# Optimization experiments

Measured on AMD Instinct MI355X. Metric: run time of the kernel, lower is better.

Reference implementation:

```python
import jax, jax.numpy as jnp
import numpy as np
from jax import lax

B, L, N_NODES, N_SEQ = 256, 15360, 16, 64


def _lstm_layer(x, wih, whh, bih, bhh):
    # x: (B, T, I); torch gate order i, f, g, o
    H = whh.shape[1]
    b = bih + bhh
    def step(carry, xt):
        h, c = carry
        gates = xt @ wih.T + h @ whh.T + b
        i, f, g, o = jnp.split(gates, 4, axis=-1)
        c = jax.nn.sigmoid(f) * c + jax.nn.sigmoid(i) * jnp.tanh(g)
        h = jax.nn.sigmoid(o) * jnp.tanh(c)
        return (h, c), h
    h0 = jnp.zeros((x.shape[0], H), x.dtype)
    _, ys = lax.scan(step, (h0, h0), x.transpose(1, 0, 2))
    return ys.transpose(1, 0, 2)


def setup_inputs() -> dict:
    ks = iter(jax.random.split(jax.random.key(0), 64))
    def rn(shape, scale=1.0):
        return (jax.random.normal(next(ks), shape) * scale).astype(jnp.float32)
    d = {"x": rn((B, 1, L))}
    chs = [1, 16, 32, 64]
    for i in range(3):
        cin, cout = chs[i], chs[i + 1]
        s = 1.0 / np.sqrt(cin * 5)
        d[f"cw{i}"] = rn((cout, cin, 5), s)
        d[f"cb{i}"] = rn((cout,), s)
        d[f"bng{i}"] = jnp.ones((cout,), jnp.float32)
        d[f"bnb{i}"] = jnp.zeros((cout,), jnp.float32)
        d[f"bnm{i}"] = jnp.zeros((cout,), jnp.float32)
        d[f"bnv{i}"] = jnp.ones((cout,), jnp.float32)
    Hh = 64
    for l in range(2):
        s = 1.0 / np.sqrt(Hh)
        d[f"wih{l}"] = rn((4 * Hh, 64), s)
        d[f"whh{l}"] = rn((4 * Hh, Hh), s)
        d[f"bih{l}"] = rn((4 * Hh,), s)
        d[f"bhh{l}"] = rn((4 * Hh,), s)
    gin = [256, 64, 64]
    for l in range(3):
        s = 1.0 / np.sqrt(gin[l])
        d[f"gw{l}"] = rn((64, gin[l]), s)
        d[f"gb{l}"] = rn((64,), s)
    d["clw"] = rn((5, 64), 0.125)
    d["clb"] = rn((5,), 0.125)
    return d


def reference(x, cw0, cb0, bng0, bnb0, bnm0, bnv0, cw1, cb1, bng1, bnb1, bnm1, bnv1, cw2, cb2, bng2, bnb2, bnm2, bnv2, wih0, whh0, bih0, bhh0, wih1, whh1, bih1, bhh1, gw0, gb0, gw1, gb1, gw2, gb2, clw, clb):
    h = x
    # CNN: [Conv1d(k=5,p=2) -> BN(eval) -> ReLU -> MaxPool(2)] x 3
    for cw, cb, g, b, m, v in ((cw0, cb0, bng0, bnb0, bnm0, bnv0),
                               (cw1, cb1, bng1, bnb1, bnm1, bnv1),
                               (cw2, cb2, bng2, bnb2, bnm2, bnv2)):
        h = lax.conv_general_dilated(h, cw, (1,), [(2, 2)], dimension_numbers=("NCH", "OIH", "NCH")) + cb[None, :, None]
        h = g[None, :, None] * (h - m[None, :, None]) * lax.rsqrt(v[None, :, None] + 1e-5) + b[None, :, None]
        h = jax.nn.relu(h)
        Bq, Cq, Lq = h.shape
        h = h.reshape(Bq, Cq, Lq // 2, 2).max(-1)
    # AdaptiveAvgPool1d(64): length divisible by 64 -> exact mean bins
    Bq, Cq, Lq = h.shape
    h = h.reshape(Bq, Cq, N_SEQ, Lq // N_SEQ).mean(-1)
    h = h.transpose(0, 2, 1)  # (B, 64, 64) = (batch, seq, channels)
    # 2-layer LSTM (dropout is identity in eval)
    h = _lstm_layer(h, wih0, whh0, bih0, bhh0)
    h = _lstm_layer(h, wih1, whh1, bih1, bhh1)
    # Graph builder: Pearson-style correlation + value thresholding
    Hf = h.reshape(Bq, -1)
    fpn = Hf.shape[1] // N_NODES  # 256 features per node
    nf = Hf[:, :N_NODES * fpn].reshape(Bq, N_NODES, fpn)
    cen = nf - nf.mean(-1, keepdims=True)
    nrm = cen / (jnp.std(cen, axis=-1, ddof=1, keepdims=True) + 1e-8)
    C = jnp.einsum("bnf,bmf->bnm", nrm, nrm) / fpn  # (B, N, N)
    Cf = C.reshape(Bq, -1)
    k = min(max(1, int((100.0 - 25.0) / 100.0 * Cf.shape[1])), Cf.shape[1] - 1)
    thr = jnp.sort(Cf, axis=1)[:, k - 1]  # torch.kthvalue(k)
    eye = jnp.eye(N_NODES, dtype=C.dtype)
    adj = (C > thr[:, None, None]).astype(C.dtype) * (1.0 - eye)
    # GCN: x = ReLU(W (x + A x) + b), 3 layers, then max over nodes
    g = nf
    for gw, gb in ((gw0, gb0), (gw1, gb1), (gw2, gb2)):
        g = jax.nn.relu((g + jnp.einsum("bnm,bmf->bnf", adj, g)) @ gw.T + gb)
    emb = g.max(axis=1)
    return emb @ clw.T + clb
```

## Files before the change

kernel.cpp:

```cpp
#include <hip/hip_runtime.h>
#include <math.h>

typedef __attribute__((ext_vector_type(2))) float v2f;

__global__ __launch_bounds__(256) void prep_weights_kernel(
    const float* __restrict__ cw0, const float* __restrict__ cb0,
    const float* __restrict__ bng0, const float* __restrict__ bnb0,
    const float* __restrict__ bnm0, const float* __restrict__ bnv0,
    const float* __restrict__ cw1, const float* __restrict__ cb1,
    const float* __restrict__ bng1, const float* __restrict__ bnb1,
    const float* __restrict__ bnm1, const float* __restrict__ bnv1,
    const float* __restrict__ cw2, const float* __restrict__ cb2,
    const float* __restrict__ bng2, const float* __restrict__ bnb2,
    const float* __restrict__ bnm2, const float* __restrict__ bnv2,
    float* __restrict__ wt1, float* __restrict__ b1,
    float* __restrict__ wt2, float* __restrict__ b2,
    float* __restrict__ w0f, float* __restrict__ b0f)
{
    int tid = threadIdx.x;
    for (int i = tid; i < 2560; i += 256) {
        int co = i & 31, r = i >> 5, t = r % 5, ci = r / 5;
        float s = bng1[co] * rsqrtf(bnv1[co] + 1e-5f);
        wt1[i] = cw1[(co * 16 + ci) * 5 + t] * s;
    }
    if (tid < 32) {
        float s = bng1[tid] * rsqrtf(bnv1[tid] + 1e-5f);
        b1[tid] = (cb1[tid] - bnm1[tid]) * s + bnb1[tid];
    }
    for (int i = tid; i < 10240; i += 256) {
        int co = i & 63, r = i >> 6, t = r % 5, ci = r / 5;
        float s = bng2[co] * rsqrtf(bnv2[co] + 1e-5f);
        wt2[i] = cw2[(co * 32 + ci) * 5 + t] * s;
    }
    if (tid < 64) {
        float s = bng2[tid] * rsqrtf(bnv2[tid] + 1e-5f);
        b2[tid] = (cb2[tid] - bnm2[tid]) * s + bnb2[tid];
    }
    if (tid < 80) {
        int co = tid / 5;
        float s = bng0[co] * rsqrtf(bnv0[co] + 1e-5f);
        w0f[tid] = cw0[tid] * s;
    }
    if (tid < 16) {
        float s = bng0[tid] * rsqrtf(bnv0[tid] + 1e-5f);
        b0f[tid] = (cb0[tid] - bnm0[tid]) * s + bnb0[tid];
    }
}

__global__ __launch_bounds__(256) void convall_kernel(
    const float* __restrict__ x,
    const float* __restrict__ w0f, const float* __restrict__ b0f,
    const float* __restrict__ wt1, const float* __restrict__ b1,
    const float* __restrict__ wt2, const float* __restrict__ b2,
    float* __restrict__ xs)
{
    __shared__ float raw[512];
    __shared__ float U[8320];
    int b = blockIdx.y, bx = blockIdx.x, tid = threadIdx.x;
    const float* xb = x + (size_t)b * 15360;
    {
        int base = 480 * bx - 14;
        for (int i = tid; i < 508; i += 256) {
            int g = base + i;
            raw[i] = (g >= 0 && g < 15360) ? xb[g] : 0.f;
        }
    }
    __syncthreads();
    {
        int ci0 = tid >> 4, sub = tid & 15;
        float w0 = w0f[ci0*5+0], w1 = w0f[ci0*5+1], w2 = w0f[ci0*5+2],
              w3 = w0f[ci0*5+3], w4 = w0f[ci0*5+4];
        float bb = b0f[ci0];
        int r0g = 240 * bx - 6;
        for (int p = sub; p < 252; p += 16) {
            int r = r0g + p;
            float v = 0.f;
            if (r >= 0 && r < 7680) {
                int i0 = 2 * p;
                float c0 = raw[i0],   c1 = raw[i0+1], c2 = raw[i0+2],
                      c3 = raw[i0+3], c4 = raw[i0+4], c5 = raw[i0+5];
                float s0 = fmaf(w0,c0, fmaf(w1,c1, fmaf(w2,c2, fmaf(w3,c3, w4*c4))));
                float s1 = fmaf(w0,c1, fmaf(w1,c2, fmaf(w2,c3, fmaf(w3,c4, w4*c5))));
                v = fmaxf(fmaxf(s0, s1) + bb, 0.f);
            }
            U[ci0 * 256 + p] = v;
        }
    }
    __syncthreads();
    {
        int cg = tid >> 7, jj = tid & 127;
        int cgu = __builtin_amdgcn_readfirstlane(cg);
        { int co = tid >> 3, c = 124 + (tid & 7); U[4096 + co * 132 + c] = 0.f; }
        if (jj < 124) {
            const float* wb = wt1 + cgu * 16;
            v2f a0[8], a1[8];
#pragma unroll
            for (int q = 0; q < 8; ++q) { a0[q] = (v2f){0.f,0.f}; a1[q] = (v2f){0.f,0.f}; }
#pragma unroll 4
            for (int ci = 0; ci < 16; ++ci) {
                const float2* xr = reinterpret_cast<const float2*>(&U[ci * 256]);
                float2 xA = xr[jj], xB = xr[jj + 1], xC = xr[jj + 2];
                float xv[6] = { xA.x, xA.y, xB.x, xB.y, xC.x, xC.y };
#pragma unroll
                for (int t = 0; t < 5; ++t) {
                    const v2f* wp2 = reinterpret_cast<const v2f*>(wb + (ci * 5 + t) * 32);
                    v2f va = { xv[t], xv[t] };
                    v2f vc = { xv[t + 1], xv[t + 1] };
#pragma unroll
                    for (int q2 = 0; q2 < 8; ++q2) {
                        v2f w = wp2[q2];
                        a0[q2] = __builtin_elementwise_fma(w, va, a0[q2]);
                        a1[q2] = __builtin_elementwise_fma(w, vc, a1[q2]);
                    }
                }
            }
            int q = 120 * bx - 2 + jj;
            bool ok = (q >= 0 && q < 3840);
#pragma unroll
            for (int q2 = 0; q2 < 8; ++q2) {
#pragma unroll
                for (int cpp = 0; cpp < 2; ++cpp) {
                    int qq = 2 * q2 + cpp;
                    int co = cgu * 16 + qq;
                    float val = 0.f;
                    if (ok) val = fmaxf(fmaxf(a0[q2][cpp], a1[q2][cpp]) + b1[co], 0.f);
                    U[4096 + co * 132 + jj] = val;
                }
            }
        }
    }
    __syncthreads();
    {
        int cg = tid >> 6, jj = tid & 63;
        int cgu = __builtin_amdgcn_readfirstlane(cg);
        const float* wb = wt2 + cgu * 16;
        v2f a0[8], a1[8];
#pragma unroll
        for (int q = 0; q < 8; ++q) { a0[q] = (v2f){0.f,0.f}; a1[q] = (v2f){0.f,0.f}; }
#pragma unroll 4
        for (int ci = 0; ci < 32; ++ci) {
            const float2* xr = reinterpret_cast<const float2*>(&U[4096 + ci * 132]);
            float2 xA = xr[jj], xB = xr[jj + 1], xC = xr[jj + 2];
            float xv[6] = { xA.x, xA.y, xB.x, xB.y, xC.x, xC.y };
#pragma unroll
            for (int t = 0; t < 5; ++t) {
                const v2f* wp2 = reinterpret_cast<const v2f*>(wb + (ci * 5 + t) * 64);
                v2f va = { xv[t], xv[t] };
                v2f vc = { xv[t + 1], xv[t + 1] };
#pragma unroll
                for (int q2 = 0; q2 < 8; ++q2) {
                    v2f w = wp2[q2];
                    a0[q2] = __builtin_elementwise_fma(w, va, a0[q2]);
                    a1[q2] = __builtin_elementwise_fma(w, vc, a1[q2]);
                }
            }
        }
        __syncthreads();
        if (jj < 60) {
#pragma unroll
            for (int q2 = 0; q2 < 8; ++q2) {
#pragma unroll
                for (int cpp = 0; cpp < 2; ++cpp) {
                    int qq = 2 * q2 + cpp;
                    int co = cgu * 16 + qq;
                    float m = fmaxf(a0[q2][cpp], a1[q2][cpp]) + b2[co];
                    U[co * 61 + jj] = fmaxf(m, 0.f);
                }
            }
        }
    }
    __syncthreads();
    if (tid < 128) {
        int co = tid & 63, bin = tid >> 6;
        const float* r = U + co * 61 + bin * 30;
        float s = 0.f;
#pragma unroll
        for (int k = 0; k < 30; ++k) s += r[k];
        xs[((size_t)b * 64 + (bx * 2 + bin)) * 64 + co] = s * (1.f / 30.f);
    }
}

__global__ __launch_bounds__(256) void lstm_kernel(
    const float* __restrict__ xseq,
    const float* __restrict__ wih0, const float* __restrict__ whh0,
    const float* __restrict__ bih0, const float* __restrict__ bhh0,
    const float* __restrict__ wih1, const float* __restrict__ whh1,
    const float* __restrict__ bih1, const float* __restrict__ bhh1,
    float* __restrict__ hseq)
{
    __shared__ float xb[64][64];
    __shared__ float xg[64][256];
    __shared__ float gb4[4][64];
    __shared__ float hb[64];
    int b = blockIdx.x;
    int tid = threadIdx.x;
    int wv = tid >> 6, ln = tid & 63;
    for (int i = tid; i < 4096; i += 256) xb[i >> 6][i & 63] = xseq[(size_t)b * 4096 + i];
    __syncthreads();
    float wr[64];
    for (int layer = 0; layer < 2; ++layer) {
        const float* wih = layer ? wih1 : wih0;
        const float* whh = layer ? whh1 : whh0;
        float bias = layer ? (bih1[tid] + bhh1[tid]) : (bih0[tid] + bhh0[tid]);
#pragma unroll
        for (int k4 = 0; k4 < 16; ++k4) {
            float4 v = reinterpret_cast<const float4*>(wih + (size_t)tid * 64)[k4];
            wr[k4 * 4 + 0] = v.x; wr[k4 * 4 + 1] = v.y;
            wr[k4 * 4 + 2] = v.z; wr[k4 * 4 + 3] = v.w;
        }
        for (int t = 0; t < 64; ++t) {
            float s0 = bias, s1 = 0.f, s2 = 0.f, s3 = 0.f;
#pragma unroll
            for (int k4 = 0; k4 < 16; ++k4) {
                float4 xv4 = *reinterpret_cast<const float4*>(&xb[t][k4 * 4]);
                s0 = fmaf(wr[k4 * 4 + 0], xv4.x, s0);
                s1 = fmaf(wr[k4 * 4 + 1], xv4.y, s1);
                s2 = fmaf(wr[k4 * 4 + 2], xv4.z, s2);
                s3 = fmaf(wr[k4 * 4 + 3], xv4.w, s3);
            }
            xg[t][tid] = (s0 + s1) + (s2 + s3);
        }
#pragma unroll
        for (int k4 = 0; k4 < 16; ++k4) {
            float4 v = reinterpret_cast<const float4*>(whh + (size_t)tid * 64)[k4];
            wr[k4 * 4 + 0] = v.x; wr[k4 * 4 + 1] = v.y;
            wr[k4 * 4 + 2] = v.z; wr[k4 * 4 + 3] = v.w;
        }
        if (tid < 64) hb[tid] = 0.f;
        float c = 0.f;
        __syncthreads();
        for (int t = 0; t < 64; ++t) {
            float s0 = xg[t][tid], s1 = 0.f, s2 = 0.f, s3 = 0.f;
#pragma unroll
            for (int k4 = 0; k4 < 16; ++k4) {
                float4 hv4 = *reinterpret_cast<const float4*>(&hb[k4 * 4]);
                s0 = fmaf(wr[k4 * 4 + 0], hv4.x, s0);
                s1 = fmaf(wr[k4 * 4 + 1], hv4.y, s1);
                s2 = fmaf(wr[k4 * 4 + 2], hv4.z, s2);
                s3 = fmaf(wr[k4 * 4 + 3], hv4.w, s3);
            }
            float acc = (s0 + s1) + (s2 + s3);
            float a;
            if (wv == 2) a = tanhf(acc);
            else         a = 1.f / (1.f + __expf(-acc));
            gb4[wv][ln] = a;
            __syncthreads();
            float gi = gb4[0][ln], gf = gb4[1][ln], gg = gb4[2][ln], go = gb4[3][ln];
            c = fmaf(gf, c, gi * gg);
            float h = go * tanhf(c);
            if (wv == 0) {
                hb[ln] = h;
                if (layer == 0) xb[t][ln] = h;
                else hseq[((size_t)b * 64 + t) * 64 + ln] = h;
            }
            __syncthreads();
        }
    }
}

__global__ __launch_bounds__(256) void graph_kernel(
    const float* __restrict__ hseq,
    const float* __restrict__ gw0, const float* __restrict__ gb0,
    const float* __restrict__ gw1, const float* __restrict__ gb1,
    const float* __restrict__ gw2, const float* __restrict__ gb2,
    const float* __restrict__ clw, const float* __restrict__ clb,
    float* __restrict__ out)
{
    __shared__ float nf[16][257];
    __shared__ float sb[16][257];
    __shared__ float red[16][17];
    __shared__ float mean[16], rstd[16];
    __shared__ float C[256];
    __shared__ float adj[16][16];
    __shared__ float thrv;
    __shared__ float bufA[16][65], bufB[16][65], bufC[16][65];
    __shared__ float emb[64];
    int b = blockIdx.x, tid = threadIdx.x;
    for (int i = tid; i < 4096; i += 256) nf[i >> 8][i & 255] = hseq[(size_t)b * 4096 + i];
    __syncthreads();
    int nd = tid >> 4, sub = tid & 15;
    {
        float s = 0.f;
        for (int f = sub; f < 256; f += 16) s += nf[nd][f];
        red[nd][sub] = s;
    }
    __syncthreads();
    if (tid < 16) {
        float m = 0.f;
        for (int i = 0; i < 16; ++i) m += red[tid][i];
        mean[tid] = m * (1.f / 256.f);
    }
    __syncthreads();
    {
        float mu = mean[nd];
        float ss = 0.f;
        for (int f = sub; f < 256; f += 16) { float d = nf[nd][f] - mu; ss = fmaf(d, d, ss); }
        red[nd][sub] = ss;
    }
    __syncthreads();
    if (tid < 16) {
        float m = 0.f;
        for (int i = 0; i < 16; ++i) m += red[tid][i];
        rstd[tid] = 1.f / (sqrtf(m * (1.f / 255.f)) + 1e-8f);
    }
    __syncthreads();
    for (int i = tid; i < 4096; i += 256) {
        int n = i >> 8, f = i & 255;
        sb[n][f] = (nf[n][f] - mean[n]) * rstd[n];
    }
    __syncthreads();
    {
        int n = tid >> 4, m = tid & 15;
        float a0 = 0, a1 = 0, a2 = 0, a3 = 0;
        for (int f = 0; f < 256; f += 4) {
            a0 = fmaf(sb[n][f + 0], sb[m][f + 0], a0);
            a1 = fmaf(sb[n][f + 1], sb[m][f + 1], a1);
            a2 = fmaf(sb[n][f + 2], sb[m][f + 2], a2);
            a3 = fmaf(sb[n][f + 3], sb[m][f + 3], a3);
        }
        C[tid] = ((a0 + a1) + (a2 + a3)) * (1.f / 256.f);
    }
    __syncthreads();
    {
        float v = C[tid];
        int cnt = 0, eq = 0;
        for (int j2 = 0; j2 < 256; ++j2) {
            float vj = C[j2];
            cnt += (vj < v);
            eq  += (vj == v);
        }
        if (cnt <= 191 && 191 < cnt + eq) thrv = v;
    }
    __syncthreads();
    {
        int n = tid >> 4, m = tid & 15;
        adj[n][m] = (C[tid] > thrv && n != m) ? 1.f : 0.f;
    }
    __syncthreads();
    for (int i = tid; i < 4096; i += 256) {
        int n = i >> 8, f = i & 255;
        float acc = nf[n][f];
#pragma unroll
        for (int m = 0; m < 16; ++m) acc = fmaf(adj[n][m], nf[m][f], acc);
        sb[n][f] = acc;
    }
    __syncthreads();
    for (int i = tid; i < 1024; i += 256) {
        int n = i >> 6, o = i & 63;
        const float4* wr4 = reinterpret_cast<const float4*>(gw0 + (size_t)o * 256);
        float acc = gb0[o];
        for (int f4 = 0; f4 < 64; ++f4) {
            float4 wv = wr4[f4];
            int f = f4 * 4;
            acc = fmaf(sb[n][f + 0], wv.x, acc);
            acc = fmaf(sb[n][f + 1], wv.y, acc);
            acc = fmaf(sb[n][f + 2], wv.z, acc);
            acc = fmaf(sb[n][f + 3], wv.w, acc);
        }
        bufA[n][o] = fmaxf(acc, 0.f);
    }
    __syncthreads();
    for (int i = tid; i < 1024; i += 256) {
        int n = i >> 6, f = i & 63;
        float acc = bufA[n][f];
#pragma unroll
        for (int m = 0; m < 16; ++m) acc = fmaf(adj[n][m], bufA[m][f], acc);
        bufB[n][f] = acc;
    }
    __syncthreads();
    for (int i = tid; i < 1024; i += 256) {
        int n = i >> 6, o = i & 63;
        const float4* wr4 = reinterpret_cast<const float4*>(gw1 + (size_t)o * 64);
        float acc = gb1[o];
        for (int f4 = 0; f4 < 16; ++f4) {
            float4 wv = wr4[f4];
            int f = f4 * 4;
            acc = fmaf(bufB[n][f + 0], wv.x, acc);
            acc = fmaf(bufB[n][f + 1], wv.y, acc);
            acc = fmaf(bufB[n][f + 2], wv.z, acc);
            acc = fmaf(bufB[n][f + 3], wv.w, acc);
        }
        bufC[n][o] = fmaxf(acc, 0.f);
    }
    __syncthreads();
    for (int i = tid; i < 1024; i += 256) {
        int n = i >> 6, f = i & 63;
        float acc = bufC[n][f];
#pragma unroll
        for (int m = 0; m < 16; ++m) acc = fmaf(adj[n][m], bufC[m][f], acc);
        bufA[n][f] = acc;
    }
    __syncthreads();
    for (int i = tid; i < 1024; i += 256) {
        int n = i >> 6, o = i & 63;
        const float4* wr4 = reinterpret_cast<const float4*>(gw2 + (size_t)o * 64);
        float acc = gb2[o];
        for (int f4 = 0; f4 < 16; ++f4) {
            float4 wv = wr4[f4];
            int f = f4 * 4;
            acc = fmaf(bufA[n][f + 0], wv.x, acc);
            acc = fmaf(bufA[n][f + 1], wv.y, acc);
            acc = fmaf(bufA[n][f + 2], wv.z, acc);
            acc = fmaf(bufA[n][f + 3], wv.w, acc);
        }
        bufB[n][o] = fmaxf(acc, 0.f);
    }
    __syncthreads();
    if (tid < 64) {
        float mx = bufB[0][tid];
#pragma unroll
        for (int n = 1; n < 16; ++n) mx = fmaxf(mx, bufB[n][tid]);
        emb[tid] = mx;
    }
    __syncthreads();
    if (tid < 5) {
        float acc = clb[tid];
#pragma unroll
        for (int o = 0; o < 64; ++o) acc = fmaf(emb[o], clw[tid * 64 + o], acc);
        out[(size_t)b * 5 + tid] = acc;
    }
}

extern "C" void kernel_launch(void* const* d_in, const int* in_sizes, int n_in,
                              void* d_out, int out_size, void* d_ws, size_t ws_size,
                              hipStream_t stream)
{
    const float* x    = (const float*)d_in[0];
    const float* cw0  = (const float*)d_in[1];
    const float* cb0  = (const float*)d_in[2];
    const float* bng0 = (const float*)d_in[3];
    const float* bnb0 = (const float*)d_in[4];
    const float* bnm0 = (const float*)d_in[5];
    const float* bnv0 = (const float*)d_in[6];
    const float* cw1  = (const float*)d_in[7];
    const float* cb1  = (const float*)d_in[8];
    const float* bng1 = (const float*)d_in[9];
    const float* bnb1 = (const float*)d_in[10];
    const float* bnm1 = (const float*)d_in[11];
    const float* bnv1 = (const float*)d_in[12];
    const float* cw2  = (const float*)d_in[13];
    const float* cb2  = (const float*)d_in[14];
    const float* bng2 = (const float*)d_in[15];
    const float* bnb2 = (const float*)d_in[16];
    const float* bnm2 = (const float*)d_in[17];
    const float* bnv2 = (const float*)d_in[18];
    const float* wih0 = (const float*)d_in[19];
    const float* whh0 = (const float*)d_in[20];
    const float* bih0 = (const float*)d_in[21];
    const float* bhh0 = (const float*)d_in[22];
    const float* wih1 = (const float*)d_in[23];
    const float* whh1 = (const float*)d_in[24];
    const float* bih1 = (const float*)d_in[25];
    const float* bhh1 = (const float*)d_in[26];
    const float* gw0  = (const float*)d_in[27];
    const float* gb0  = (const float*)d_in[28];
    const float* gw1  = (const float*)d_in[29];
    const float* gb1  = (const float*)d_in[30];
    const float* gw2  = (const float*)d_in[31];
    const float* gb2  = (const float*)d_in[32];
    const float* clw  = (const float*)d_in[33];
    const float* clb  = (const float*)d_in[34];

    float* xs  = (float*)d_ws;
    float* hs  = xs + 1048576;
    float* wt1 = hs + 1048576;
    float* b1  = wt1 + 2560;
    float* wt2 = b1 + 32;
    float* b2  = wt2 + 10240;
    float* w0f = b2 + 64;
    float* b0f = w0f + 80;

    prep_weights_kernel<<<1, 256, 0, stream>>>(
        cw0, cb0, bng0, bnb0, bnm0, bnv0,
        cw1, cb1, bng1, bnb1, bnm1, bnv1,
        cw2, cb2, bng2, bnb2, bnm2, bnv2,
        wt1, b1, wt2, b2, w0f, b0f);
    convall_kernel<<<dim3(32, 256), 256, 0, stream>>>(x, w0f, b0f, wt1, b1, wt2, b2, xs);
    lstm_kernel<<<256, 256, 0, stream>>>(xs, wih0, whh0, bih0, bhh0,
                                         wih1, whh1, bih1, bhh1, hs);
    graph_kernel<<<256, 256, 0, stream>>>(hs, gw0, gb0, gw1, gb1, gw2, gb2,
                                          clw, clb, (float*)d_out);
}
```

Baseline: 478.0 us.

## Fuse LSTM and graph kernels, remove per-step barrier, shrink conv LDS

Merges the LSTM and graph/GCN kernels into one, so the layer-2 hidden sequence stays in shared memory and the global round trip and a launch go away. Each wave now keeps its own copy of h and double-buffers the gate buffer, which drops the second __syncthreads per timestep. The conv kernel packs its shared buffers tighter (raw aliased into U, smaller strides, clamped reads) to use less LDS and possibly raise occupancy. The tighter strides may add bank conflicts, and the merged kernel's larger shared footprint may lower occupancy.

After: 469.0 us. No clear change (-1.9%).

```diff
diff --git a/kernel.cpp b/kernel.cpp
--- a/kernel.cpp
+++ b/kernel.cpp
@@ -54,8 +54,8 @@
     const float* __restrict__ wt2, const float* __restrict__ b2,
     float* __restrict__ xs)
 {
-    __shared__ float raw[512];
-    __shared__ float U[8320];
+    __shared__ float U[8096];
+    float* raw = &U[4064];
     int b = blockIdx.y, bx = blockIdx.x, tid = threadIdx.x;
     const float* xb = x + (size_t)b * 15360;
     {
@@ -83,14 +83,14 @@
                 float s1 = fmaf(w0,c1, fmaf(w1,c2, fmaf(w2,c3, fmaf(w3,c4, w4*c5))));
                 v = fmaxf(fmaxf(s0, s1) + bb, 0.f);
             }
-            U[ci0 * 256 + p] = v;
+            U[ci0 * 254 + p] = v;
         }
     }
     __syncthreads();
     {
         int cg = tid >> 7, jj = tid & 127;
         int cgu = __builtin_amdgcn_readfirstlane(cg);
-        { int co = tid >> 3, c = 124 + (tid & 7); U[4096 + co * 132 + c] = 0.f; }
+        if (tid < 64) { int co = tid >> 1, c = 124 + (tid & 1); U[4064 + co * 126 + c] = 0.f; }
         if (jj < 124) {
             const float* wb = wt1 + cgu * 16;
             v2f a0[8], a1[8];
@@ -98,7 +98,7 @@
             for (int q = 0; q < 8; ++q) { a0[q] = (v2f){0.f,0.f}; a1[q] = (v2f){0.f,0.f}; }
 #pragma unroll 4
             for (int ci = 0; ci < 16; ++ci) {
-                const float2* xr = reinterpret_cast<const float2*>(&U[ci * 256]);
+                const float2* xr = reinterpret_cast<const float2*>(&U[ci * 254]);
                 float2 xA = xr[jj], xB = xr[jj + 1], xC = xr[jj + 2];
                 float xv[6] = { xA.x, xA.y, xB.x, xB.y, xC.x, xC.y };
 #pragma unroll
@@ -124,7 +124,7 @@
                     int co = cgu * 16 + qq;
                     float val = 0.f;
                     if (ok) val = fmaxf(fmaxf(a0[q2][cpp], a1[q2][cpp]) + b1[co], 0.f);
-                    U[4096 + co * 132 + jj] = val;
+                    U[4064 + co * 126 + jj] = val;
                 }
             }
         }
@@ -132,6 +132,7 @@
     __syncthreads();
     {
         int cg = tid >> 6, jj = tid & 63;
+        int jje = (jj < 59) ? jj : 59;
         int cgu = __builtin_amdgcn_readfirstlane(cg);
         const float* wb = wt2 + cgu * 16;
         v2f a0[8], a1[8];
@@ -139,8 +140,8 @@
         for (int q = 0; q < 8; ++q) { a0[q] = (v2f){0.f,0.f}; a1[q] = (v2f){0.f,0.f}; }
 #pragma unroll 4
         for (int ci = 0; ci < 32; ++ci) {
-            const float2* xr = reinterpret_cast<const float2*>(&U[4096 + ci * 132]);
-            float2 xA = xr[jj], xB = xr[jj + 1], xC = xr[jj + 2];
+            const float2* xr = reinterpret_cast<const float2*>(&U[4064 + ci * 126]);
+            float2 xA = xr[jje], xB = xr[jje + 1], xC = xr[jje + 2];
             float xv[6] = { xA.x, xA.y, xB.x, xB.y, xC.x, xC.y };
 #pragma unroll
             for (int t = 0; t < 5; ++t) {
@@ -176,22 +177,26 @@
         float s = 0.f;
 #pragma unroll
         for (int k = 0; k < 30; ++k) s += r[k];
-        xs[((size_t)b * 64 + (bx * 2 + bin)) * 64 + co] = s * (1.f / 30.f);
+        xs[((size_t)b * 64 + (blockIdx.x * 2 + bin)) * 64 + co] = s * (1.f / 30.f);
     }
 }
 
-__global__ __launch_bounds__(256) void lstm_kernel(
+__global__ __launch_bounds__(256) void lstmgraph_kernel(
     const float* __restrict__ xseq,
     const float* __restrict__ wih0, const float* __restrict__ whh0,
     const float* __restrict__ bih0, const float* __restrict__ bhh0,
     const float* __restrict__ wih1, const float* __restrict__ whh1,
     const float* __restrict__ bih1, const float* __restrict__ bhh1,
-    float* __restrict__ hseq)
+    const float* __restrict__ gw0, const float* __restrict__ gb0,
+    const float* __restrict__ gw1, const float* __restrict__ gb1,
+    const float* __restrict__ gw2, const float* __restrict__ gb2,
+    const float* __restrict__ clw, const float* __restrict__ clb,
+    float* __restrict__ out)
 {
     __shared__ float xb[64][64];
-    __shared__ float xg[64][256];
-    __shared__ float gb4[4][64];
-    __shared__ float hb[64];
+    __shared__ float xg[16384];
+    __shared__ float gbuf[2][4][64];
+    __shared__ float hbw[4][64];
     int b = blockIdx.x;
     int tid = threadIdx.x;
     int wv = tid >> 6, ln = tid & 63;
@@ -218,7 +223,7 @@
                 s2 = fmaf(wr[k4 * 4 + 2], xv4.z, s2);
                 s3 = fmaf(wr[k4 * 4 + 3], xv4.w, s3);
             }
-            xg[t][tid] = (s0 + s1) + (s2 + s3);
+            xg[t * 256 + tid] = (s0 + s1) + (s2 + s3);
         }
 #pragma unroll
         for (int k4 = 0; k4 < 16; ++k4) {
@@ -226,14 +231,14 @@
             wr[k4 * 4 + 0] = v.x; wr[k4 * 4 + 1] = v.y;
             wr[k4 * 4 + 2] = v.z; wr[k4 * 4 + 3] = v.w;
         }
-        if (tid < 64) hb[tid] = 0.f;
+        hbw[wv][ln] = 0.f;
         float c = 0.f;
         __syncthreads();
         for (int t = 0; t < 64; ++t) {
-            float s0 = xg[t][tid], s1 = 0.f, s2 = 0.f, s3 = 0.f;
+            float s0 = xg[t * 256 + tid], s1 = 0.f, s2 = 0.f, s3 = 0.f;
 #pragma unroll
             for (int k4 = 0; k4 < 16; ++k4) {
-                float4 hv4 = *reinterpret_cast<const float4*>(&hb[k4 * 4]);
+                float4 hv4 = *reinterpret_cast<const float4*>(&hbw[wv][k4 * 4]);
                 s0 = fmaf(wr[k4 * 4 + 0], hv4.x, s0);
                 s1 = fmaf(wr[k4 * 4 + 1], hv4.y, s1);
                 s2 = fmaf(wr[k4 * 4 + 2], hv4.z, s2);
@@ -243,80 +248,73 @@
             float a;
             if (wv == 2) a = tanhf(acc);
             else         a = 1.f / (1.f + __expf(-acc));
-            gb4[wv][ln] = a;
+            gbuf[t & 1][wv][ln] = a;
             __syncthreads();
-            float gi = gb4[0][ln], gf = gb4[1][ln], gg = gb4[2][ln], go = gb4[3][ln];
+            float gi = gbuf[t & 1][0][ln], gf = gbuf[t & 1][1][ln],
+                  gg = gbuf[t & 1][2][ln], go = gbuf[t & 1][3][ln];
             c = fmaf(gf, c, gi * gg);
             float h = go * tanhf(c);
-            if (wv == 0) {
-                hb[ln] = h;
-                if (layer == 0) xb[t][ln] = h;
-                else hseq[((size_t)b * 64 + t) * 64 + ln] = h;
-            }
-            __syncthreads();
-        }
-    }
-}
-
-__global__ __launch_bounds__(256) void graph_kernel(
-    const float* __restrict__ hseq,
-    const float* __restrict__ gw0, const float* __restrict__ gb0,
-    const float* __restrict__ gw1, const float* __restrict__ gb1,
-    const float* __restrict__ gw2, const float* __restrict__ gb2,
-    const float* __restrict__ clw, const float* __restrict__ clb,
-    float* __restrict__ out)
-{
-    __shared__ float nf[16][257];
-    __shared__ float sb[16][257];
-    __shared__ float red[16][17];
-    __shared__ float mean[16], rstd[16];
-    __shared__ float C[256];
-    __shared__ float adj[16][16];
-    __shared__ float thrv;
-    __shared__ float bufA[16][65], bufB[16][65], bufC[16][65];
-    __shared__ float emb[64];
-    int b = blockIdx.x, tid = threadIdx.x;
-    for (int i = tid; i < 4096; i += 256) nf[i >> 8][i & 255] = hseq[(size_t)b * 4096 + i];
+            hbw[wv][ln] = h;
+            if (wv == 0) xb[t][ln] = h;
+        }
+        __syncthreads();
+    }
+    float* nf   = xg;
+    float* sb   = xg + 4112;
+    float* red  = xg + 8224;
+    float* mean = xg + 8496;
+    float* rstd = xg + 8512;
+    float* C    = xg + 8528;
+    float* adj  = xg + 8784;
+    float* thrv = xg + 9040;
+    float* bufA = xg + 9044;
+    float* bufB = xg + 10084;
+    float* bufC = xg + 11124;
+    float* emb  = xg + 12164;
+    for (int i = tid; i < 4096; i += 256) {
+        int n = i >> 8, f = i & 255;
+        nf[n * 257 + f] = xb[4 * n + (f >> 6)][f & 63];
+    }
     __syncthreads();
     int nd = tid >> 4, sub = tid & 15;
     {
         float s = 0.f;
-        for (int f = sub; f < 256; f += 16) s += nf[nd][f];
-        red[nd][sub] = s;
+        for (int f = sub; f < 256; f += 16) s += nf[nd * 257 + f];
+        red[nd * 17 + sub] = s;
     }
     __syncthreads();
     if (tid < 16) {
         float m = 0.f;
-        for (int i = 0; i < 16; ++i) m += red[tid][i];
+        for (int i = 0; i < 16; ++i) m += red[tid * 17 + i];
         mean[tid] = m * (1.f / 256.f);
     }
     __syncthreads();
     {
         float mu = mean[nd];
         float ss = 0.f;
-        for (int f = sub; f < 256; f += 16) { float d = nf[nd][f] - mu; ss = fmaf(d, d, ss); }
-        red[nd][sub] = ss;
+        for (int f = sub; f < 256; f += 16) { float d = nf[nd * 257 + f] - mu; ss = fmaf(d, d, ss); }
+        red[nd * 17 + sub] = ss;
     }
     __syncthreads();
     if (tid < 16) {
         float m = 0.f;
-        for (int i = 0; i < 16; ++i) m += red[tid][i];
+        for (int i = 0; i < 16; ++i) m += red[tid * 17 + i];
         rstd[tid] = 1.f / (sqrtf(m * (1.f / 255.f)) + 1e-8f);
     }
     __syncthreads();
     for (int i = tid; i < 4096; i += 256) {
         int n = i >> 8, f = i & 255;
-        sb[n][f] = (nf[n][f] - mean[n]) * rstd[n];
+        sb[n * 257 + f] = (nf[n * 257 + f] - mean[n]) * rstd[n];
     }
     __syncthreads();
     {
         int n = tid >> 4, m = tid & 15;
         float a0 = 0, a1 = 0, a2 = 0, a3 = 0;
         for (int f = 0; f < 256; f += 4) {
-            a0 = fmaf(sb[n][f + 0], sb[m][f + 0], a0);
-            a1 = fmaf(sb[n][f + 1], sb[m][f + 1], a1);
-            a2 = fmaf(sb[n][f + 2], sb[m][f + 2], a2);
-            a3 = fmaf(sb[n][f + 3], sb[m][f + 3], a3);
+            a0 = fmaf(sb[n * 257 + f + 0], sb[m * 257 + f + 0], a0);
+            a1 = fmaf(sb[n * 257 + f + 1], sb[m * 257 + f + 1], a1);
+            a2 = fmaf(sb[n * 257 + f + 2], sb[m * 257 + f + 2], a2);
+            a3 = fmaf(sb[n * 257 + f + 3], sb[m * 257 + f + 3], a3);
         }
         C[tid] = ((a0 + a1) + (a2 + a3)) * (1.f / 256.f);
     }
@@ -329,20 +327,20 @@
             cnt += (vj < v);
             eq  += (vj == v);
         }
-        if (cnt <= 191 && 191 < cnt + eq) thrv = v;
+        if (cnt <= 191 && 191 < cnt + eq) thrv[0] = v;
     }
     __syncthreads();
     {
         int n = tid >> 4, m = tid & 15;
-        adj[n][m] = (C[tid] > thrv && n != m) ? 1.f : 0.f;
+        adj[tid] = (C[tid] > thrv[0] && n != m) ? 1.f : 0.f;
     }
     __syncthreads();
     for (int i = tid; i < 4096; i += 256) {
         int n = i >> 8, f = i & 255;
-        float acc = nf[n][f];
-#pragma unroll
-        for (int m = 0; m < 16; ++m) acc = fmaf(adj[n][m], nf[m][f], acc);
-        sb[n][f] = acc;
+        float acc = nf[n * 257 + f];
+#pragma unroll
+        for (int m = 0; m < 16; ++m) acc = fmaf(adj[n * 16 + m], nf[m * 257 + f], acc);
+        sb[n * 257 + f] = acc;
     }
     __syncthreads();
     for (int i = tid; i < 1024; i += 256) {
@@ -350,22 +348,22 @@
         const float4* wr4 = reinterpret_cast<const float4*>(gw0 + (size_t)o * 256);
         float acc = gb0[o];
         for (int f4 = 0; f4 < 64; ++f4) {
-            float4 wv = wr4[f4];
+            float4 wv4 = wr4[f4];
             int f = f4 * 4;
-            acc = fmaf(sb[n][f + 0], wv.x, acc);
-            acc = fmaf(sb[n][f + 1], wv.y, acc);
-            acc = fmaf(sb[n][f + 2], wv.z, acc);
-            acc = fmaf(sb[n][f + 3], wv.w, acc);
-        }
-        bufA[n][o] = fmaxf(acc, 0.f);
+            acc = fmaf(sb[n * 257 + f + 0], wv4.x, acc);
+            acc = fmaf(sb[n * 257 + f + 1], wv4.y, acc);
+            acc = fmaf(sb[n * 257 + f + 2], wv4.z, acc);
+            acc = fmaf(sb[n * 257 + f + 3], wv4.w, acc);
+        }
+        bufA[n * 65 + o] = fmaxf(acc, 0.f);
     }
     __syncthreads();
     for (int i = tid; i < 1024; i += 256) {
         int n = i >> 6, f = i & 63;
-        float acc = bufA[n][f];
-#pragma unroll
-        for (int m = 0; m < 16; ++m) acc = fmaf(adj[n][m], bufA[m][f], acc);
-        bufB[n][f] = acc;
+        float acc = bufA[n * 65 + f];
+#pragma unroll
+        for (int m = 0; m < 16; ++m) acc = fmaf(adj[n * 16 + m], bufA[m * 65 + f], acc);
+        bufB[n * 65 + f] = acc;
     }
     __syncthreads();
     for (int i = tid; i < 1024; i += 256) {
@@ -373,22 +371,22 @@
         const float4* wr4 = reinterpret_cast<const float4*>(gw1 + (size_t)o * 64);
         float acc = gb1[o];
         for (int f4 = 0; f4 < 16; ++f4) {
-            float4 wv = wr4[f4];
+            float4 wv4 = wr4[f4];
             int f = f4 * 4;
-            acc = fmaf(bufB[n][f + 0], wv.x, acc);
-            acc = fmaf(bufB[n][f + 1], wv.y, acc);
-            acc = fmaf(bufB[n][f + 2], wv.z, acc);
-            acc = fmaf(bufB[n][f + 3], wv.w, acc);
-        }
-        bufC[n][o] = fmaxf(acc, 0.f);
+            acc = fmaf(bufB[n * 65 + f + 0], wv4.x, acc);
+            acc = fmaf(bufB[n * 65 + f + 1], wv4.y, acc);
+            acc = fmaf(bufB[n * 65 + f + 2], wv4.z, acc);
+            acc = fmaf(bufB[n * 65 + f + 3], wv4.w, acc);
+        }
+        bufC[n * 65 + o] = fmaxf(acc, 0.f);
     }
     __syncthreads();
     for (int i = tid; i < 1024; i += 256) {
         int n = i >> 6, f = i & 63;
-        float acc = bufC[n][f];
-#pragma unroll
-        for (int m = 0; m < 16; ++m) acc = fmaf(adj[n][m], bufC[m][f], acc);
-        bufA[n][f] = acc;
+        float acc = bufC[n * 65 + f];
+#pragma unroll
+        for (int m = 0; m < 16; ++m) acc = fmaf(adj[n * 16 + m], bufC[m * 65 + f], acc);
+        bufA[n * 65 + f] = acc;
     }
     __syncthreads();
     for (int i = tid; i < 1024; i += 256) {
@@ -396,20 +394,20 @@
         const float4* wr4 = reinterpret_cast<const float4*>(gw2 + (size_t)o * 64);
         float acc = gb2[o];
         for (int f4 = 0; f4 < 16; ++f4) {
-            float4 wv = wr4[f4];
+            float4 wv4 = wr4[f4];
             int f = f4 * 4;
-            acc = fmaf(bufA[n][f + 0], wv.x, acc);
-            acc = fmaf(bufA[n][f + 1], wv.y, acc);
-            acc = fmaf(bufA[n][f + 2], wv.z, acc);
-            acc = fmaf(bufA[n][f + 3], wv.w, acc);
-        }
-        bufB[n][o] = fmaxf(acc, 0.f);
+            acc = fmaf(bufA[n * 65 + f + 0], wv4.x, acc);
+            acc = fmaf(bufA[n * 65 + f + 1], wv4.y, acc);
+            acc = fmaf(bufA[n * 65 + f + 2], wv4.z, acc);
+            acc = fmaf(bufA[n * 65 + f + 3], wv4.w, acc);
+        }
+        bufB[n * 65 + o] = fmaxf(acc, 0.f);
     }
     __syncthreads();
     if (tid < 64) {
-        float mx = bufB[0][tid];
-#pragma unroll
-        for (int n = 1; n < 16; ++n) mx = fmaxf(mx, bufB[n][tid]);
+        float mx = bufB[0 * 65 + tid];
+#pragma unroll
+        for (int n = 1; n < 16; ++n) mx = fmaxf(mx, bufB[n * 65 + tid]);
         emb[tid] = mx;
     }
     __syncthreads();
@@ -462,8 +460,7 @@
     const float* clb  = (const float*)d_in[34];
 
     float* xs  = (float*)d_ws;
-    float* hs  = xs + 1048576;
-    float* wt1 = hs + 1048576;
+    float* wt1 = xs + 1048576;
     float* b1  = wt1 + 2560;
     float* wt2 = b1 + 32;
     float* b2  = wt2 + 10240;
@@ -476,8 +473,8 @@
         cw2, cb2, bng2, bnb2, bnm2, bnv2,
         wt1, b1, wt2, b2, w0f, b0f);
     convall_kernel<<<dim3(32, 256), 256, 0, stream>>>(x, w0f, b0f, wt1, b1, wt2, b2, xs);
-    lstm_kernel<<<256, 256, 0, stream>>>(xs, wih0, whh0, bih0, bhh0,
-                                         wih1, whh1, bih1, bhh1, hs);
-    graph_kernel<<<256, 256, 0, stream>>>(hs, gw0, gb0, gw1, gb1, gw2, gb2,
-                                          clw, clb, (float*)d_out);
+    lstmgraph_kernel<<<256, 256, 0, stream>>>(xs, wih0, whh0, bih0, bhh0,
+                                              wih1, whh1, bih1, bhh1,
+                                              gw0, gb0, gw1, gb1, gw2, gb2,
+                                              clw, clb, (float*)d_out);
 }
```
